# Optimization experiments

Hardware: AMD Instinct MI355X
Metric: run time of the kernel (lower is better)

The kernel has to match this reference:

```python
import jax, jax.numpy as jnp
import numpy as np

H = 16          # head_count
D = 1024        # model_dim
DPH = D // H    # dim_per_head


def setup_inputs() -> dict:
    key0 = jax.random.key(0)
    ks = jax.random.split(key0, 13)
    B, S = 4, 2048
    scale = 1.0 / np.sqrt(D)
    inp = {
        "key": jax.random.normal(ks[0], (B, S, D), jnp.float32),
        "value": jax.random.normal(ks[1], (B, S, D), jnp.float32),
        "query": jax.random.normal(ks[2], (B, S, D), jnp.float32),
        "mask": jax.random.randint(ks[3], (B, S, S), 0, 2).astype(jnp.bool_),
        "Wq": jax.random.normal(ks[4], (D, D), jnp.float32) * scale,
        "bq": jnp.zeros((D,), jnp.float32),
        "Wk": jax.random.normal(ks[5], (D, D), jnp.float32) * scale,
        "bk": jnp.zeros((D,), jnp.float32),
        "Wv": jax.random.normal(ks[6], (D, D), jnp.float32) * scale,
        "bv": jnp.zeros((D,), jnp.float32),
        "Wo": jax.random.normal(ks[7], (D, D), jnp.float32) * scale,
        "bo": jnp.zeros((D,), jnp.float32),
    }
    return inp


def _shape(x, B):
    # [B, S, D] -> [B, H, S, DPH]
    return x.reshape(B, -1, H, DPH).transpose(0, 2, 1, 3)


def reference(key, value, query, mask, Wq, bq, Wk, bk, Wv, bv, Wo, bo):
    B, S, _ = key.shape
    k_up = _shape(key @ Wk + bk, B)                       # [B,H,S,DPH]
    v_up = _shape(value @ Wv + bv, B)                     # [B,H,S,DPH]
    q_up = _shape(query @ Wq + bq, B) / jnp.sqrt(jnp.asarray(DPH, key.dtype))
    scores = jnp.einsum('bhqd,bhkd->bhqk', q_up, k_up)    # [B,H,S,S]
    scores = jnp.where(mask[:, None, :, :], jnp.asarray(-1e18, scores.dtype), scores)
    attn = jax.nn.softmax(scores, axis=-1)                # dropout = identity (eval)
    context = jnp.einsum('bhqk,bhkd->bhqd', attn, v_up)   # [B,H,S,DPH]
    context = context.transpose(0, 2, 1, 3).reshape(B, S, H * DPH)
    return context @ Wo + bo
```

## Files before the change

### kernel.cpp

```cpp
#include <hip/hip_runtime.h>

typedef _Float16 half8 __attribute__((ext_vector_type(8)));
typedef _Float16 half4 __attribute__((ext_vector_type(4)));
typedef float floatx4 __attribute__((ext_vector_type(4)));
typedef float floatx16 __attribute__((ext_vector_type(16)));

#define MFMA16(A,B,C) __builtin_amdgcn_mfma_f32_16x16x32_f16((A),(B),(C),0,0,0)
#define MFMA32(A,B,C) __builtin_amdgcn_mfma_f32_32x32x16_f16((A),(B),(C),0,0,0)


__global__ __launch_bounds__(256) void maskpack(
    const int* __restrict__ m, unsigned int* __restrict__ p)
{
  const int w = blockIdx.x * 256 + threadIdx.x;
  const int b = w >> 17;
  const int rem = w & 131071;
  const int s = rem >> 6;
  const int wp = rem & 63;
  const int4* src = (const int4*)(m + (size_t)w * 32);
  unsigned int bits = 0;
#pragma unroll
  for (int j = 0; j < 8; ++j) {
    const int4 v = src[j];
    bits |= (v.x ? 1u : 0u) << (j * 4 + 0);
    bits |= (v.y ? 1u : 0u) << (j * 4 + 1);
    bits |= (v.z ? 1u : 0u) << (j * 4 + 2);
    bits |= (v.w ? 1u : 0u) << (j * 4 + 3);
  }
  p[((size_t)(b * 64 + wp)) * 2048 + s] = bits;
}

__global__ __launch_bounds__(256) void wconv(
    const float* __restrict__ Wq, const float* __restrict__ Wk,
    const float* __restrict__ Wv, const float* __restrict__ Wo,
    _Float16* __restrict__ dst)
{
  const float* W = (blockIdx.z == 0) ? Wq : (blockIdx.z == 1) ? Wk
                  : (blockIdx.z == 2) ? Wv : Wo;
  _Float16* WT = dst + (size_t)blockIdx.z * 1024 * 1024;
  __shared__ float t[32][33];
  const int tx = threadIdx.x & 31;
  const int ty = threadIdx.x >> 5;
  const int k0 = blockIdx.x * 32, n0 = blockIdx.y * 32;
#pragma unroll
  for (int j = 0; j < 4; ++j)
    t[ty + j * 8][tx] = W[(size_t)(k0 + ty + j * 8) * 1024 + n0 + tx];
  __syncthreads();
#pragma unroll
  for (int j = 0; j < 4; ++j)
    WT[(size_t)(n0 + ty + j * 8) * 1024 + k0 + tx] = (_Float16)t[tx][ty + j * 8];
}

template <int OP>
__global__ __launch_bounds__(256) void gemm_k(
    const void* __restrict__ Ap, const _Float16* __restrict__ BT,
    const float* __restrict__ bias, void* __restrict__ Cp)
{
  __shared__ __align__(16) _Float16 As[128 * 64];
  __shared__ __align__(16) _Float16 Bs[128 * 64];
  const int tid = threadIdx.x;
  const int lane = tid & 63;
  const int wv = tid >> 6;
  const int m0 = blockIdx.x * 128;
  const int n0 = blockIdx.y * 128;
  const int wr = (wv >> 1) * 64;
  const int wc = (wv & 1) * 64;

  floatx4 acc[4][4];
#pragma unroll
  for (int i = 0; i < 4; ++i)
#pragma unroll
    for (int j = 0; j < 4; ++j) acc[i][j] = (floatx4){0.f, 0.f, 0.f, 0.f};

  char* AsB = (char*)As;
  char* BsB = (char*)Bs;

  for (int ko = 0; ko < 1024; ko += 64) {
#pragma unroll
    for (int r = 0; r < 4; ++r) {
      const int idx = (r * 256 + tid) * 8;
      const int row = idx >> 6;
      const int colh = idx & 63;
      const int dstb = row * 128 + ((colh * 2) ^ ((row & 7) << 4));
      if (OP == 3) {
        const _Float16* s = (const _Float16*)Ap + (size_t)(m0 + row) * 1024 + ko + colh;
        *(half8*)(AsB + dstb) = *(const half8*)s;
      } else {
        const float* s = (const float*)Ap + (size_t)(m0 + row) * 1024 + ko + colh;
        floatx4 v0 = *(const floatx4*)s;
        floatx4 v1 = *(const floatx4*)(s + 4);
        union { half8 v; unsigned int u[4]; } pk;
        pk.u[0] = __builtin_bit_cast(unsigned int, __builtin_amdgcn_cvt_pkrtz(v0[0], v0[1]));
        pk.u[1] = __builtin_bit_cast(unsigned int, __builtin_amdgcn_cvt_pkrtz(v0[2], v0[3]));
        pk.u[2] = __builtin_bit_cast(unsigned int, __builtin_amdgcn_cvt_pkrtz(v1[0], v1[1]));
        pk.u[3] = __builtin_bit_cast(unsigned int, __builtin_amdgcn_cvt_pkrtz(v1[2], v1[3]));
        *(half8*)(AsB + dstb) = pk.v;
      }
      const _Float16* bs = BT + (size_t)(n0 + row) * 1024 + ko + colh;
      *(half8*)(BsB + dstb) = *(const half8*)bs;
    }
    __syncthreads();
#pragma unroll
    for (int kk = 0; kk < 64; kk += 32) {
      half8 af[4], bf[4];
#pragma unroll
      for (int mi = 0; mi < 4; ++mi) {
        const int row = wr + mi * 16 + (lane & 15);
        const int cb = (kk + (lane >> 4) * 8) * 2;
        af[mi] = *(const half8*)(AsB + row * 128 + (cb ^ ((row & 7) << 4)));
      }
#pragma unroll
      for (int ni = 0; ni < 4; ++ni) {
        const int row = wc + ni * 16 + (lane & 15);
        const int cb = (kk + (lane >> 4) * 8) * 2;
        bf[ni] = *(const half8*)(BsB + row * 128 + (cb ^ ((row & 7) << 4)));
      }
#pragma unroll
      for (int mi = 0; mi < 4; ++mi)
#pragma unroll
        for (int ni = 0; ni < 4; ++ni)
          acc[mi][ni] = MFMA16(af[mi], bf[ni], acc[mi][ni]);
    }
    __syncthreads();
  }

#pragma unroll
  for (int ni = 0; ni < 4; ++ni) {
    const int nn = n0 + wc + ni * 16 + (lane & 15);
    const float bvv = bias[nn];
#pragma unroll
    for (int mi = 0; mi < 4; ++mi) {
      floatx4 c = acc[mi][ni];
#pragma unroll
      for (int i = 0; i < 4; ++i) {
        const int mm = m0 + wr + mi * 16 + (lane >> 4) * 4 + i;
        float val = c[i] + bvv;
        if (OP == 0) val *= 0.1803368801111204f;
        if (OP == 0 || OP == 1) {
          _Float16* o = (_Float16*)Cp;
          const size_t off =
              ((size_t)((mm >> 11) * 16 + (nn >> 6)) * 2048 + (mm & 2047)) * 64 + (nn & 63);
          o[off] = (_Float16)val;
        } else if (OP == 2) {
          _Float16* o = (_Float16*)Cp;
          const int mmp = (mm & ~0xC) | ((mm & 4) << 1) | ((mm & 8) >> 1);
          const size_t off =
              ((size_t)((mm >> 11) * 16 + (nn >> 6)) * 64 + (nn & 63)) * 2048 + (mmp & 2047);
          o[off] = (_Float16)val;
        } else {
          float* o = (float*)Cp;
          o[(size_t)mm * 1024 + nn] = val;
        }
      }
    }
  }
}

__global__ __launch_bounds__(512) void attn_k(
    const _Float16* __restrict__ q_up, const _Float16* __restrict__ k_up,
    const _Float16* __restrict__ vT, const unsigned int* __restrict__ pmaskT,
    _Float16* __restrict__ ctx)
{
  const int tid = threadIdx.x;
  const int lane = tid & 63;
  const int wv = tid >> 6;
  const int bid = blockIdx.x;
  const int xcd = bid & 7;
  const int slot = bid >> 3;
  const int bh = xcd * 8 + (slot & 7);
  const int qc = slot >> 3;
  const int b = bh >> 4;
  const int h = bh & 15;
  const int l31 = lane & 31;
  const int hi = lane >> 5;
  const int qw = qc * 256 + wv * 32;

  __shared__ __align__(16) _Float16 Kl[2][32 * 64];
  __shared__ __align__(16) _Float16 Vl[2][64 * 32];

  const _Float16* qb = q_up + ((size_t)bh * 2048 + qw) * 64;
  const _Float16* kb = k_up + (size_t)bh * 2048 * 64;
  const _Float16* vb = vT + (size_t)bh * 64 * 2048;
  const unsigned int* mbase = pmaskT + (size_t)(b * 64) * 2048 + qw + l31;

  const bool isK = tid < 256;
  const int st = isK ? tid : tid - 256;
  const int vrow = st >> 2, vseg = st & 3;
  const int sOff = isK
      ? (((st & 7) >> 1) * 1024 + (st >> 3) * 32 + (st & 1) * 16)
      : ((vseg >> 1) * 2048 + vrow * 32 + (vseg & 1) * 16);
  const _Float16* gsrc = isK ? (kb + (size_t)st * 8)
                             : (vb + (size_t)vrow * 2048 + vseg * 8);
  const int gstride = isK ? 2048 : 32;
  char* Lbase = isK ? (char*)Kl : (char*)Vl;
  char* KB = (char*)Kl;
  char* VB = (char*)Vl;

  half8 qf[4];
#pragma unroll
  for (int kk = 0; kk < 4; ++kk)
    qf[kk] = *(const half8*)(qb + (size_t)l31 * 64 + kk * 16 + hi * 8);

  floatx16 O[2];
#pragma unroll
  for (int dt = 0; dt < 2; ++dt)
#pragma unroll
    for (int r = 0; r < 16; ++r) O[dt][r] = 0.f;
  float lsum = 0.f;

  floatx16 zero16;
#pragma unroll
  for (int r = 0; r < 16; ++r) zero16[r] = 0.f;

  half8 stg;

  auto COMPUTE = [&](int buf, int t) {
    const unsigned int mw = mbase[(size_t)t * 2048];
    half8 kf[4];
#pragma unroll
    for (int kk = 0; kk < 4; ++kk)
      kf[kk] = *(const half8*)(KB + buf * 4096 + kk * 1024 + l31 * 32 + hi * 16);
    half8 vf[2][2];
#pragma unroll
    for (int dt = 0; dt < 2; ++dt)
#pragma unroll
      for (int kk2 = 0; kk2 < 2; ++kk2)
        vf[dt][kk2] = *(const half8*)(VB + buf * 4096 + kk2 * 2048 +
                                      (dt * 32 + l31) * 32 + hi * 16);

    floatx16 s;
    __builtin_amdgcn_s_setprio(1);
    {
      floatx16 a;
      a = MFMA32(kf[0], qf[0], zero16);
      a = MFMA32(kf[1], qf[1], a);
      a = MFMA32(kf[2], qf[2], a);
      s = MFMA32(kf[3], qf[3], a);
    }
    __builtin_amdgcn_s_setprio(0);

    const unsigned int mh = mw >> (4 * hi);
    float e[16];
#pragma unroll
    for (int m = 0; m < 4; ++m) {
      const unsigned int bm = mh >> (8 * m);
#pragma unroll
      for (int j = 0; j < 4; ++j)
        e[4 * m + j] = ((bm >> j) & 1u) ? 0.f : __builtin_amdgcn_exp2f(s[4 * m + j]);
    }
    float u0 = (e[0] + e[1]) + (e[2] + e[3]);
    float u1 = (e[4] + e[5]) + (e[6] + e[7]);
    float u2 = (e[8] + e[9]) + (e[10] + e[11]);
    float u3 = (e[12] + e[13]) + (e[14] + e[15]);
    lsum += (u0 + u1) + (u2 + u3);

    union { half8 v; unsigned int u[4]; } p0, p1;
    p0.u[0] = __builtin_bit_cast(unsigned int, __builtin_amdgcn_cvt_pkrtz(e[0], e[1]));
    p0.u[1] = __builtin_bit_cast(unsigned int, __builtin_amdgcn_cvt_pkrtz(e[2], e[3]));
    p0.u[2] = __builtin_bit_cast(unsigned int, __builtin_amdgcn_cvt_pkrtz(e[4], e[5]));
    p0.u[3] = __builtin_bit_cast(unsigned int, __builtin_amdgcn_cvt_pkrtz(e[6], e[7]));
    p1.u[0] = __builtin_bit_cast(unsigned int, __builtin_amdgcn_cvt_pkrtz(e[8], e[9]));
    p1.u[1] = __builtin_bit_cast(unsigned int, __builtin_amdgcn_cvt_pkrtz(e[10], e[11]));
    p1.u[2] = __builtin_bit_cast(unsigned int, __builtin_amdgcn_cvt_pkrtz(e[12], e[13]));
    p1.u[3] = __builtin_bit_cast(unsigned int, __builtin_amdgcn_cvt_pkrtz(e[14], e[15]));
    __builtin_amdgcn_s_setprio(1);
#pragma unroll
    for (int dt = 0; dt < 2; ++dt) {
      O[dt] = MFMA32(vf[dt][0], p0.v, O[dt]);
      O[dt] = MFMA32(vf[dt][1], p1.v, O[dt]);
    }
    __builtin_amdgcn_s_setprio(0);
  };

  stg = *(const half8*)gsrc;
  *(half8*)(Lbase + sOff) = stg;
  stg = *(const half8*)(gsrc + gstride);
  __syncthreads();

#pragma unroll 1
  for (int t = 0; t < 64; t += 2) {
    {
      *(half8*)(Lbase + 4096 + sOff) = stg;
      const int tn = (t + 2 < 64) ? t + 2 : 0;
      stg = *(const half8*)(gsrc + (size_t)tn * gstride);
      COMPUTE(0, t);
      __syncthreads();
    }
    {
      *(half8*)(Lbase + sOff) = stg;
      const int tn = (t + 3 < 64) ? t + 3 : 0;
      stg = *(const half8*)(gsrc + (size_t)tn * gstride);
      COMPUTE(1, t + 1);
      __syncthreads();
    }
  }

  {
    const float tot = lsum + __shfl_xor(lsum, 32);
    const float inv = 1.f / tot;
    const size_t rowb = ((size_t)(b * 2048 + qw + l31)) * 1024 + h * 64;
#pragma unroll
    for (int dt = 0; dt < 2; ++dt) {
#pragma unroll
      for (int m = 0; m < 4; ++m) {
        half4 w4;
        w4[0] = (_Float16)(O[dt][4 * m + 0] * inv);
        w4[1] = (_Float16)(O[dt][4 * m + 1] * inv);
        w4[2] = (_Float16)(O[dt][4 * m + 2] * inv);
        w4[3] = (_Float16)(O[dt][4 * m + 3] * inv);
        *(half4*)(ctx + rowb + dt * 32 + 8 * m + 4 * hi) = w4;
      }
    }
  }
}

extern "C" void kernel_launch(void* const* d_in, const int* in_sizes, int n_in,
                              void* d_out, int out_size, void* d_ws, size_t ws_size,
                              hipStream_t stream) {
  const float* key   = (const float*)d_in[0];
  const float* value = (const float*)d_in[1];
  const float* query = (const float*)d_in[2];
  const int*   mask  = (const int*)d_in[3];
  const float* Wq = (const float*)d_in[4];
  const float* bq = (const float*)d_in[5];
  const float* Wk = (const float*)d_in[6];
  const float* bk = (const float*)d_in[7];
  const float* Wv = (const float*)d_in[8];
  const float* bv = (const float*)d_in[9];
  const float* Wo = (const float*)d_in[10];
  const float* bo = (const float*)d_in[11];

  _Float16* wsp = (_Float16*)d_ws;
  _Float16* WT   = wsp;
  _Float16* q_up = wsp + (size_t)4 * 1024 * 1024;
  _Float16* k_up = q_up + (size_t)8192 * 1024;
  _Float16* vT   = k_up + (size_t)8192 * 1024;
  _Float16* ctx  = vT + (size_t)8192 * 1024;
  unsigned int* pmaskT = (unsigned int*)(ctx + (size_t)8192 * 1024);

  maskpack<<<dim3(2048), 256, 0, stream>>>(mask, pmaskT);
  wconv<<<dim3(32, 32, 4), 256, 0, stream>>>(Wq, Wk, Wv, Wo, WT);
  gemm_k<0><<<dim3(64, 8), 256, 0, stream>>>(query, WT, bq, q_up);
  gemm_k<1><<<dim3(64, 8), 256, 0, stream>>>(key, WT + (size_t)1024 * 1024, bk, k_up);
  gemm_k<2><<<dim3(64, 8), 256, 0, stream>>>(value, WT + (size_t)2 * 1024 * 1024, bv, vT);
  attn_k<<<dim3(512), 512, 0, stream>>>(q_up, k_up, vT, pmaskT, ctx);
  gemm_k<3><<<dim3(64, 8), 256, 0, stream>>>(ctx, WT + (size_t)3 * 1024 * 1024, bo, (float*)d_out);
}
```

Baseline: 252.0 us.

## Split attention over two KV halves and merge partials in a reduction kernel

The attention kernel now launches twice as many blocks, and each block processes half of the key/value sequence. Each half writes an unnormalized fp16 partial context plus per-row softmax sums. A new elementwise kernel adds the two partials and divides by the combined sum to produce the context. The aim is more parallelism and occupancy on the GPU. The cost is an extra launch and extra global-memory traffic for the partials. The merge also assumes both halves share the same softmax normalization offset, since no per-half max rescaling is applied.

```diff
diff --git a/kernel.cpp b/kernel.cpp
--- a/kernel.cpp
+++ b/kernel.cpp
@@ -159,21 +159,24 @@
 __global__ __launch_bounds__(512) void attn_k(
     const _Float16* __restrict__ q_up, const _Float16* __restrict__ k_up,
     const _Float16* __restrict__ vT, const unsigned int* __restrict__ pmaskT,
-    _Float16* __restrict__ ctx)
+    _Float16* __restrict__ P0, _Float16* __restrict__ P1,
+    float* __restrict__ Lsum)
 {
   const int tid = threadIdx.x;
   const int lane = tid & 63;
   const int wv = tid >> 6;
   const int bid = blockIdx.x;
   const int xcd = bid & 7;
-  const int slot = bid >> 3;
-  const int bh = xcd * 8 + (slot & 7);
-  const int qc = slot >> 3;
+  const int rest = bid >> 3;
+  const int bh = xcd * 8 + (rest & 7);
+  const int qc = (rest >> 3) & 7;
+  const int kvh = rest >> 6;
   const int b = bh >> 4;
   const int h = bh & 15;
   const int l31 = lane & 31;
   const int hi = lane >> 5;
   const int qw = qc * 256 + wv * 32;
+  const int t0 = kvh * 32;
 
   __shared__ __align__(16) _Float16 Kl[2][32 * 64];
   __shared__ __align__(16) _Float16 Vl[2][64 * 32];
@@ -272,23 +275,24 @@
     __builtin_amdgcn_s_setprio(0);
   };
 
-  stg = *(const half8*)gsrc;
+  stg = *(const half8*)(gsrc + (size_t)t0 * gstride);
   *(half8*)(Lbase + sOff) = stg;
-  stg = *(const half8*)(gsrc + gstride);
+  stg = *(const half8*)(gsrc + (size_t)(t0 + 1) * gstride);
   __syncthreads();
 
 #pragma unroll 1
-  for (int t = 0; t < 64; t += 2) {
+  for (int tt = 0; tt < 32; tt += 2) {
+    const int t = t0 + tt;
     {
       *(half8*)(Lbase + 4096 + sOff) = stg;
-      const int tn = (t + 2 < 64) ? t + 2 : 0;
+      const int tn = (tt + 2 < 32) ? t + 2 : t0;
       stg = *(const half8*)(gsrc + (size_t)tn * gstride);
       COMPUTE(0, t);
       __syncthreads();
     }
     {
       *(half8*)(Lbase + sOff) = stg;
-      const int tn = (t + 3 < 64) ? t + 3 : 0;
+      const int tn = (tt + 3 < 32) ? t + 3 : t0;
       stg = *(const half8*)(gsrc + (size_t)tn * gstride);
       COMPUTE(1, t + 1);
       __syncthreads();
@@ -297,21 +301,43 @@
 
   {
     const float tot = lsum + __shfl_xor(lsum, 32);
-    const float inv = 1.f / tot;
+    _Float16* Pp = kvh ? P1 : P0;
     const size_t rowb = ((size_t)(b * 2048 + qw + l31)) * 1024 + h * 64;
 #pragma unroll
     for (int dt = 0; dt < 2; ++dt) {
 #pragma unroll
       for (int m = 0; m < 4; ++m) {
         half4 w4;
-        w4[0] = (_Float16)(O[dt][4 * m + 0] * inv);
-        w4[1] = (_Float16)(O[dt][4 * m + 1] * inv);
-        w4[2] = (_Float16)(O[dt][4 * m + 2] * inv);
-        w4[3] = (_Float16)(O[dt][4 * m + 3] * inv);
-        *(half4*)(ctx + rowb + dt * 32 + 8 * m + 4 * hi) = w4;
-      }
-    }
-  }
+        w4[0] = (_Float16)O[dt][4 * m + 0];
+        w4[1] = (_Float16)O[dt][4 * m + 1];
+        w4[2] = (_Float16)O[dt][4 * m + 2];
+        w4[3] = (_Float16)O[dt][4 * m + 3];
+        *(half4*)(Pp + rowb + dt * 32 + 8 * m + 4 * hi) = w4;
+      }
+    }
+    if (hi == 0)
+      Lsum[(size_t)kvh * 131072 + (size_t)bh * 2048 + qw + l31] = tot;
+  }
+}
+
+__global__ __launch_bounds__(256) void attnred(
+    const _Float16* __restrict__ P1, const float* __restrict__ Lsum,
+    _Float16* __restrict__ ctx)
+{
+  const size_t i8 = ((size_t)blockIdx.x * 256 + threadIdx.x) * 8;
+  const int row = (int)(i8 >> 10);
+  const int col = (int)(i8 & 1023);
+  const int bq = row & 2047;
+  const int bh = (row >> 11) * 16 + (col >> 6);
+  const size_t li = (size_t)bh * 2048 + bq;
+  const float inv = 1.f / (Lsum[li] + Lsum[131072 + li]);
+  half8 a = *(const half8*)(ctx + i8);
+  half8 c = *(const half8*)(P1 + i8);
+  half8 o;
+#pragma unroll
+  for (int j = 0; j < 8; ++j)
+    o[j] = (_Float16)(((float)a[j] + (float)c[j]) * inv);
+  *(half8*)(ctx + i8) = o;
 }
 
 extern "C" void kernel_launch(void* const* d_in, const int* in_sizes, int n_in,
@@ -337,12 +363,15 @@
   _Float16* vT   = k_up + (size_t)8192 * 1024;
   _Float16* ctx  = vT + (size_t)8192 * 1024;
   unsigned int* pmaskT = (unsigned int*)(ctx + (size_t)8192 * 1024);
+  _Float16* P1 = (_Float16*)(pmaskT + (size_t)524288);
+  float* Lsum = (float*)(P1 + (size_t)8192 * 1024);
 
   maskpack<<<dim3(2048), 256, 0, stream>>>(mask, pmaskT);
   wconv<<<dim3(32, 32, 4), 256, 0, stream>>>(Wq, Wk, Wv, Wo, WT);
   gemm_k<0><<<dim3(64, 8), 256, 0, stream>>>(query, WT, bq, q_up);
   gemm_k<1><<<dim3(64, 8), 256, 0, stream>>>(key, WT + (size_t)1024 * 1024, bk, k_up);
   gemm_k<2><<<dim3(64, 8), 256, 0, stream>>>(value, WT + (size_t)2 * 1024 * 1024, bv, vT);
-  attn_k<<<dim3(512), 512, 0, stream>>>(q_up, k_up, vT, pmaskT, ctx);
+  attn_k<<<dim3(1024), 512, 0, stream>>>(q_up, k_up, vT, pmaskT, ctx, P1, Lsum);
+  attnred<<<dim3(4096), 256, 0, stream>>>(P1, Lsum, ctx);
   gemm_k<3><<<dim3(64, 8), 256, 0, stream>>>(ctx, WT + (size_t)3 * 1024 * 1024, bo, (float*)d_out);
 }
```

After: 266.5 us. 5.7% more time.
